# Optimization experiments

Measured on AMD Instinct MI355X. Metric: run time of the kernel, lower is better.

Reference implementation:

```python
import jax, jax.numpy as jnp
import numpy as np

B, N, F_IN, HID, OUT, NHEADS = 16, 1024, 64, 64, 64, 4
TAXI = 512        # get_Parameter('taxi_size') from the original repo (node split point)
ALPHA = 0.2       # LeakyReLU negative slope


def setup_inputs() -> dict:
    key = jax.random.key(0)
    ks = jax.random.split(key, 8)
    x = jax.random.normal(ks[0], (B, N, F_IN), dtype=jnp.float32)
    # multiplicative binary mask (mostly ones so softmax rows are well-conditioned)
    mask = (jax.random.uniform(ks[1], (N, N)) > 0.1).astype(jnp.float32)
    s_in = 1.0 / np.sqrt(F_IN)
    s_cat = 1.0 / np.sqrt(NHEADS * HID)
    W1 = jax.random.normal(ks[2], (NHEADS, F_IN, HID), jnp.float32) * s_in
    W2 = jax.random.normal(ks[3], (NHEADS, F_IN, HID), jnp.float32) * s_in
    a = jax.random.normal(ks[4], (NHEADS, 2 * HID), jnp.float32) * 0.1
    W1o = jax.random.normal(ks[5], (NHEADS * HID, OUT), jnp.float32) * s_cat
    W2o = jax.random.normal(ks[6], (NHEADS * HID, OUT), jnp.float32) * s_cat
    ao = jax.random.normal(ks[7], (2 * OUT,), jnp.float32) * 0.1
    return dict(x=x, mask=mask, W1=W1, W2=W2, a=a, W1o=W1o, W2o=W2o, ao=ao)


def _gat_layer(x, mask, W1, W2, a, out_dim):
    # x: [B,N,F]; W1,W2: [F,out_dim]; a: [2*out_dim]
    # node-group-split linear projection (taxi nodes via W1, rest via W2)
    h = jnp.concatenate([x[:, :TAXI] @ W1, x[:, TAXI:] @ W2], axis=1)  # [B,N,O]
    A1 = h @ a[:out_dim]                 # [B,N]
    A2 = h @ a[out_dim:]                 # [B,N]
    sim = A1[:, :, None] + A2[:, None, :]  # [B,N,N] additive scores
    e = jax.nn.leaky_relu(sim, ALPHA)
    e = mask[None, :, :] * e             # multiplicative mask (as in source)
    attn = jax.nn.softmax(e, axis=-1)    # [B,N,N]  (dropout omitted: eval mode)
    h_prime = jnp.einsum('bnm,bmo->bno', attn, h)
    return jax.nn.elu(h_prime), attn


def reference(x, mask, W1, W2, a, W1o, W2o, ao):
    # input dropout omitted (eval mode)
    heads = [_gat_layer(x, mask, W1[i], W2[i], a[i], HID)[0] for i in range(NHEADS)]
    xc = jnp.concatenate(heads, axis=-1)          # [B,N,NHEADS*HID]
    out, attn = _gat_layer(xc, mask, W1o, W2o, ao, OUT)
    return out, attn
```

## Files before the change

### kernel.cpp

```cpp
#include <hip/hip_runtime.h>
#include <hip/hip_bf16.h>

#define B_      16
#define N_      1024
#define ALPHA_  0.2f

typedef __attribute__((ext_vector_type(8))) __bf16 bf16x8;
typedef __attribute__((ext_vector_type(4))) float  floatx4;

__device__ __forceinline__ float eluf(float u) { return u > 0.f ? u : __expf(u) - 1.f; }

__device__ __forceinline__ floatx4 mfma_bf16(bf16x8 a, bf16x8 b, floatx4 c) {
    return __builtin_amdgcn_mfma_f32_16x16x32_bf16(a, b, c, 0, 0, 0);
}

__global__ __launch_bounds__(256) void maskbits_kernel(
    const float* __restrict__ mask, unsigned* __restrict__ bits)
{
    const int idx = blockIdx.x * 256 + threadIdx.x;
    const float* src = mask + (size_t)idx * 32;
    unsigned v = 0;
#pragma unroll
    for (int j = 0; j < 8; ++j) {
        float4 f = *(const float4*)(src + j * 4);
        v |= ((unsigned)(f.x != 0.f)) << (j * 4 + 0);
        v |= ((unsigned)(f.y != 0.f)) << (j * 4 + 1);
        v |= ((unsigned)(f.z != 0.f)) << (j * 4 + 2);
        v |= ((unsigned)(f.w != 0.f)) << (j * 4 + 3);
    }
    bits[idx] = v;
}

__global__ __launch_bounds__(256) void proj1_kernel(
    const float* __restrict__ x, const float* __restrict__ W1,
    const float* __restrict__ W2, const float* __restrict__ av,
    __bf16* __restrict__ h1t, float* __restrict__ A1, float* __restrict__ A2)
{
    const int tile = blockIdx.x, b = blockIdx.y, head = blockIdx.z;
    const int n0 = tile * 64;
    const float* W  = ((n0 < 512) ? W1 : W2) + head * 64 * 64;
    const float* ah = av + head * 128;

    __shared__ __align__(16) __bf16 xs[64][72];
    __shared__ __align__(16) __bf16 Wt[64][72];
    __shared__ __align__(16) float as_[128];

    const int tid = threadIdx.x;
    if (tid < 128) as_[tid] = ah[tid];
#pragma unroll
    for (int i = 0; i < 4; ++i) {
        int idx = i * 256 + tid;
        int r = idx >> 4, c = (idx & 15) * 4;
        float4 v = *(const float4*)(x + ((size_t)(b * N_ + n0 + r)) * 64 + c);
        xs[r][c+0] = (__bf16)v.x; xs[r][c+1] = (__bf16)v.y;
        xs[r][c+2] = (__bf16)v.z; xs[r][c+3] = (__bf16)v.w;
        float4 wv = *(const float4*)(W + (size_t)r * 64 + c);
        Wt[c+0][r] = (__bf16)wv.x; Wt[c+1][r] = (__bf16)wv.y;
        Wt[c+2][r] = (__bf16)wv.z; Wt[c+3][r] = (__bf16)wv.w;
    }
    __syncthreads();

    const int w = tid >> 6, L = tid & 63, quad = L >> 4, lo = L & 15;
    floatx4 acc[4] = {{0,0,0,0},{0,0,0,0},{0,0,0,0},{0,0,0,0}};
#pragma unroll
    for (int kc = 0; kc < 2; ++kc) {
        bf16x8 af = *(bf16x8*)&xs[16 * w + lo][kc * 32 + quad * 8];
#pragma unroll
        for (int t = 0; t < 4; ++t) {
            bf16x8 bv = *(bf16x8*)&Wt[16 * t + lo][kc * 32 + quad * 8];
            acc[t] = mfma_bf16(af, bv, acc[t]);
        }
    }

    float p1[4] = {0, 0, 0, 0}, p2[4] = {0, 0, 0, 0};
#pragma unroll
    for (int t = 0; t < 4; ++t) {
        float a1w = as_[16 * t + lo], a2w = as_[64 + 16 * t + lo];
#pragma unroll
        for (int i = 0; i < 4; ++i) { p1[i] += acc[t][i] * a1w; p2[i] += acc[t][i] * a2w; }
    }
#pragma unroll
    for (int s = 1; s < 16; s <<= 1)
#pragma unroll
        for (int i = 0; i < 4; ++i) {
            p1[i] += __shfl_xor(p1[i], s);
            p2[i] += __shfl_xor(p2[i], s);
        }
    const int bh = head * B_ + b;
    if (lo == 0) {
#pragma unroll
        for (int i = 0; i < 4; ++i) {
            int n = 16 * w + quad * 4 + i;
            A1[bh * N_ + n0 + n] = p1[i];
            A2[bh * N_ + n0 + n] = p2[i];
        }
    }

    __syncthreads();
#pragma unroll
    for (int t = 0; t < 4; ++t)
#pragma unroll
        for (int i = 0; i < 4; ++i)
            xs[16 * w + quad * 4 + i][16 * t + lo] = (__bf16)acc[t][i];
    __syncthreads();
    const int d = tid & 63, ch = tid >> 6;
    bf16x8 v0, v1;
#pragma unroll
    for (int j = 0; j < 8; ++j) v0[j] = xs[ch * 16 + j][d];
#pragma unroll
    for (int j = 0; j < 8; ++j) v1[j] = xs[ch * 16 + 8 + j][d];
    bf16x8* dst = (bf16x8*)(h1t + ((size_t)bh * 64 + d) * N_ + n0 + ch * 16);
    dst[0] = v0; dst[1] = v1;
}

__global__ __launch_bounds__(256, 4) void attn1_kernel(
    const float* __restrict__ A1g, const float* __restrict__ A2g,
    const __bf16* __restrict__ Htg, const unsigned* __restrict__ bitsG,
    __bf16* __restrict__ xc_out)
{
    const int b = blockIdx.x, head = blockIdx.y, tile = blockIdx.z;
    const int n0 = tile * 64;
    const int bh = head * B_ + b;
    const float* A2 = A2g + (size_t)bh * N_;
    const __bf16* Hglob = Htg + (size_t)bh * 64 * N_;

    __shared__ __align__(16) __bf16 Ht[2][64][72];
    __shared__ __align__(16) __bf16 ts[64][72];
    __shared__ __align__(16) float A2s[N_];
    __shared__ __align__(16) unsigned bitsS[2048];

    const int tid = threadIdx.x;
    *(float4*)&A2s[tid * 4] = *(const float4*)(A2 + tid * 4);
    {
        uint4 u0 = *(const uint4*)(bitsG + n0 * 32 + tid * 8);
        uint4 u1 = *(const uint4*)(bitsG + n0 * 32 + tid * 8 + 4);
        const int row = tid >> 2, wb0 = (tid & 3) * 8;
        bitsS[(wb0+0)*64+row] = u0.x; bitsS[(wb0+1)*64+row] = u0.y;
        bitsS[(wb0+2)*64+row] = u0.z; bitsS[(wb0+3)*64+row] = u0.w;
        bitsS[(wb0+4)*64+row] = u1.x; bitsS[(wb0+5)*64+row] = u1.y;
        bitsS[(wb0+6)*64+row] = u1.z; bitsS[(wb0+7)*64+row] = u1.w;
    }

    const int sr = tid >> 2, sq = tid & 3;
    const __bf16* hrow = Hglob + (size_t)sr * N_ + sq * 16;
    const int w = tid >> 6, L = tid & 63, quad = L >> 4, lo = L & 15;
    const int nloc = 16 * w + lo;
    const float a1r = A1g[(size_t)bh * N_ + n0 + nloc];
    const int shq = quad * 8;

    bf16x8 h0 = *(const bf16x8*)(hrow);
    bf16x8 h1 = *(const bf16x8*)(hrow + 8);
    *(bf16x8*)&Ht[0][sr][sq * 16]     = h0;
    *(bf16x8*)&Ht[0][sr][sq * 16 + 8] = h1;
    __syncthreads();

    floatx4 acc[4] = {{0,0,0,0},{0,0,0,0},{0,0,0,0},{0,0,0,0}};
    float zacc = 0.f;

    for (int mt = 0; mt < 16; ++mt) {
        const int cur = mt & 1;
        if (mt < 15) {
            h0 = *(const bf16x8*)(hrow + (mt + 1) * 64);
            h1 = *(const bf16x8*)(hrow + (mt + 1) * 64 + 8);
        }
        bf16x8 pf0, pf1;
#pragma unroll
        for (int kc = 0; kc < 2; ++kc) {
            const int mb = mt * 64 + kc * 32 + shq;
            const unsigned wbk = bitsS[(mt * 2 + kc) * 64 + nloc] >> shq;
            float4 alo = *(const float4*)&A2s[mb];
            float4 ahi = *(const float4*)&A2s[mb + 4];
            float a2v[8] = {alo.x, alo.y, alo.z, alo.w, ahi.x, ahi.y, ahi.z, ahi.w};
            float o[8];
#pragma unroll
            for (int j = 0; j < 8; ++j) {
                float s = a1r + a2v[j];
                float lr = fmaxf(s, ALPHA_ * s);
                int bm = (int)(wbk << (31 - j)) >> 31;
                lr = __int_as_float(__float_as_int(lr) & bm);
                float t = __expf(lr);
                zacc += t; o[j] = t;
            }
            bf16x8 pk = {(__bf16)o[0], (__bf16)o[1], (__bf16)o[2], (__bf16)o[3],
                         (__bf16)o[4], (__bf16)o[5], (__bf16)o[6], (__bf16)o[7]};
            if (kc == 0) pf0 = pk; else pf1 = pk;
        }
#pragma unroll
        for (int t = 0; t < 4; ++t) {
            bf16x8 bv = *(bf16x8*)&Ht[cur][16 * t + lo][shq];
            acc[t] = mfma_bf16(pf0, bv, acc[t]);
        }
#pragma unroll
        for (int t = 0; t < 4; ++t) {
            bf16x8 bv = *(bf16x8*)&Ht[cur][16 * t + lo][32 + shq];
            acc[t] = mfma_bf16(pf1, bv, acc[t]);
        }
        if (mt < 15) {
            *(bf16x8*)&Ht[cur ^ 1][sr][sq * 16]     = h0;
            *(bf16x8*)&Ht[cur ^ 1][sr][sq * 16 + 8] = h1;
            __syncthreads();
        }
    }

    zacc += __shfl_xor(zacc, 16);
    zacc += __shfl_xor(zacc, 32);
    const float invz = 1.f / zacc;
    float iz[4];
#pragma unroll
    for (int i = 0; i < 4; ++i) iz[i] = __shfl(invz, quad * 4 + i);

#pragma unroll
    for (int t = 0; t < 4; ++t)
#pragma unroll
        for (int i = 0; i < 4; ++i)
            ts[16 * w + quad * 4 + i][16 * t + lo] = (__bf16)eluf(acc[t][i] * iz[i]);
    __syncthreads();
#pragma unroll
    for (int i = 0; i < 2; ++i) {
        int cid = i * 256 + tid;
        int row = cid >> 3, c8 = (cid & 7) * 8;
        bf16x8 v = *(bf16x8*)&ts[row][c8];
        *(bf16x8*)(xc_out + ((size_t)(b * N_ + n0 + row)) * 256 + head * 64 + c8) = v;
    }
}

__global__ __launch_bounds__(256) void attn2_kernel(
    const float* __restrict__ A1g, const float* __restrict__ A2g,
    const __bf16* __restrict__ Htg, const unsigned* __restrict__ bitsG,
    float* __restrict__ out_f, float* __restrict__ attn_f)
{
    const int b = blockIdx.x, tile = blockIdx.z;
    const int n0 = tile * 32;
    const float* A2 = A2g + (size_t)b * N_;
    const __bf16* Hglob = Htg + (size_t)b * 64 * N_;

    __shared__ __align__(16) __bf16 ts2[2][32][72];
    __shared__ __align__(16) __bf16 Ht2[2][64][72];
    __shared__ __align__(16) float A2s[N_];
    __shared__ __align__(16) unsigned bitsS[1024];
    __shared__ float invz[32];

    const int tid = threadIdx.x;
    *(float4*)&A2s[tid * 4] = *(const float4*)(A2 + tid * 4);
    {
        uint4 u = *(const uint4*)(bitsG + n0 * 32 + tid * 4);
        const int row = tid >> 3, wb0 = (tid & 7) * 4;
        bitsS[(wb0+0)*32+row] = u.x; bitsS[(wb0+1)*32+row] = u.y;
        bitsS[(wb0+2)*32+row] = u.z; bitsS[(wb0+3)*32+row] = u.w;
    }

    const int r2 = tid >> 3, q2 = tid & 7;
    const float a1r = A1g[(size_t)b * N_ + n0 + r2];
    const int dr = tid >> 2, dq = tid & 3;
    const int w = tid >> 6, L = tid & 63, quad = L >> 4, lo = L & 15;
    const __bf16* hrow = Hglob + (size_t)dr * N_ + dq * 16;

    floatx4 acc2[2] = {{0,0,0,0},{0,0,0,0}};
    float zacc = 0.f;
    bf16x8 tr[16];

    __syncthreads();

    auto scores = [&](int mt) -> bf16x8 {
        const int mb = mt * 64 + q2 * 8;
        const unsigned wb = bitsS[(mt * 2 + (q2 >> 2)) * 32 + r2] >> ((q2 & 3) * 8);
        float4 alo = *(const float4*)&A2s[mb];
        float4 ahi = *(const float4*)&A2s[mb + 4];
        float a2v[8] = {alo.x, alo.y, alo.z, alo.w, ahi.x, ahi.y, ahi.z, ahi.w};
        float o[8];
#pragma unroll
        for (int j = 0; j < 8; ++j) {
            float s = a1r + a2v[j];
            float lr = fmaxf(s, ALPHA_ * s);
            int bm = (int)(wb << (31 - j)) >> 31;
            lr = __int_as_float(__float_as_int(lr) & bm);
            float t = __expf(lr);
            zacc += t; o[j] = t;
        }
        bf16x8 pk = {(__bf16)o[0], (__bf16)o[1], (__bf16)o[2], (__bf16)o[3],
                     (__bf16)o[4], (__bf16)o[5], (__bf16)o[6], (__bf16)o[7]};
        return pk;
    };

    {
        bf16x8 h0 = *(const bf16x8*)(hrow);
        bf16x8 h1 = *(const bf16x8*)(hrow + 8);
        bf16x8 pk = scores(0);
        tr[0] = pk;
        *(bf16x8*)&ts2[0][r2][q2 * 8]      = pk;
        *(bf16x8*)&Ht2[0][dr][dq * 16]     = h0;
        *(bf16x8*)&Ht2[0][dr][dq * 16 + 8] = h1;
    }
    __syncthreads();

#pragma unroll
    for (int mt = 0; mt < 16; ++mt) {
        const int cur = mt & 1;
        bf16x8 h0, h1, pk;
        if (mt < 15) {
            h0 = *(const bf16x8*)(hrow + (mt + 1) * 64);
            h1 = *(const bf16x8*)(hrow + (mt + 1) * 64 + 8);
            pk = scores(mt + 1);
            tr[mt + 1] = pk;
        }
#pragma unroll
        for (int c = 0; c < 2; ++c)
#pragma unroll
            for (int rt = 0; rt < 2; ++rt) {
                bf16x8 af = *(bf16x8*)&ts2[cur][16 * rt + lo][c * 32 + quad * 8];
                bf16x8 bv = *(bf16x8*)&Ht2[cur][16 * w + lo][c * 32 + quad * 8];
                acc2[rt] = mfma_bf16(af, bv, acc2[rt]);
            }
        if (mt < 15) {
            *(bf16x8*)&ts2[cur ^ 1][r2][q2 * 8]      = pk;
            *(bf16x8*)&Ht2[cur ^ 1][dr][dq * 16]     = h0;
            *(bf16x8*)&Ht2[cur ^ 1][dr][dq * 16 + 8] = h1;
            __syncthreads();
        }
    }

    zacc += __shfl_xor(zacc, 1);
    zacc += __shfl_xor(zacc, 2);
    zacc += __shfl_xor(zacc, 4);
    if (q2 == 0) invz[r2] = 1.f / zacc;
    __syncthreads();

#pragma unroll
    for (int rt = 0; rt < 2; ++rt)
#pragma unroll
        for (int i = 0; i < 4; ++i) {
            const int n = 16 * rt + quad * 4 + i;
            out_f[((size_t)(b * N_ + n0 + n)) * 64 + 16 * w + lo] =
                eluf(acc2[rt][i] * invz[n]);
        }

    const float iz = invz[r2];
    float* arow = attn_f + ((size_t)(b * N_ + n0 + r2)) * N_ + q2 * 8;
#pragma unroll
    for (int mt = 0; mt < 16; ++mt) {
        bf16x8 t8 = tr[mt];
        float4 f0 = make_float4((float)t8[0] * iz, (float)t8[1] * iz,
                                (float)t8[2] * iz, (float)t8[3] * iz);
        float4 f1 = make_float4((float)t8[4] * iz, (float)t8[5] * iz,
                                (float)t8[6] * iz, (float)t8[7] * iz);
        *(float4*)(arow + mt * 64)     = f0;
        *(float4*)(arow + mt * 64 + 4) = f1;
    }
}

__global__ __launch_bounds__(256) void proj2_kernel(
    const __bf16* __restrict__ xcb, const float* __restrict__ W1o,
    const float* __restrict__ W2o, const float* __restrict__ ao,
    __bf16* __restrict__ h2t, float* __restrict__ A1o, float* __restrict__ A2o)
{
    const int tile = blockIdx.x, b = blockIdx.y;
    const int n0 = tile * 64;
    const float* W = (n0 < 512) ? W1o : W2o;

    __shared__ __align__(16) __bf16 xs[64][264];
    __shared__ __align__(16) __bf16 Wt[64][264];
    __shared__ __align__(16) float as_[128];

    const int tid = threadIdx.x;
    if (tid < 128) as_[tid] = ao[tid];

#pragma unroll
    for (int i = 0; i < 8; ++i) {
        int idx = i * 256 + tid;
        int row = idx >> 5, c = (idx & 31) * 8;
        *(bf16x8*)&xs[row][c] =
            *(const bf16x8*)(xcb + ((size_t)(b * N_ + n0 + row)) * 256 + c);
    }
#pragma unroll
    for (int i = 0; i < 16; ++i) {
        int idx = i * 256 + tid;
        int k = idx >> 4, n4 = (idx & 15) * 4;
        float4 wv = *(const float4*)(W + (size_t)k * 64 + n4);
        Wt[n4 + 0][k] = (__bf16)wv.x;
        Wt[n4 + 1][k] = (__bf16)wv.y;
        Wt[n4 + 2][k] = (__bf16)wv.z;
        Wt[n4 + 3][k] = (__bf16)wv.w;
    }
    __syncthreads();

    const int w = tid >> 6, L = tid & 63, quad = L >> 4, lo = L & 15;
    floatx4 acc[4] = {{0,0,0,0},{0,0,0,0},{0,0,0,0},{0,0,0,0}};
#pragma unroll
    for (int kc = 0; kc < 8; ++kc) {
        bf16x8 af = *(bf16x8*)&xs[16 * w + lo][kc * 32 + quad * 8];
#pragma unroll
        for (int t = 0; t < 4; ++t) {
            bf16x8 bv = *(bf16x8*)&Wt[16 * t + lo][kc * 32 + quad * 8];
            acc[t] = mfma_bf16(af, bv, acc[t]);
        }
    }

    float p1[4] = {0, 0, 0, 0}, p2[4] = {0, 0, 0, 0};
#pragma unroll
    for (int t = 0; t < 4; ++t) {
        float a1w = as_[16 * t + lo], a2w = as_[64 + 16 * t + lo];
#pragma unroll
        for (int i = 0; i < 4; ++i) { p1[i] += acc[t][i] * a1w; p2[i] += acc[t][i] * a2w; }
    }
#pragma unroll
    for (int s = 1; s < 16; s <<= 1)
#pragma unroll
        for (int i = 0; i < 4; ++i) {
            p1[i] += __shfl_xor(p1[i], s);
            p2[i] += __shfl_xor(p2[i], s);
        }
    if (lo == 0) {
#pragma unroll
        for (int i = 0; i < 4; ++i) {
            int n = 16 * w + quad * 4 + i;
            A1o[b * N_ + n0 + n] = p1[i];
            A2o[b * N_ + n0 + n] = p2[i];
        }
    }

    __syncthreads();
#pragma unroll
    for (int t = 0; t < 4; ++t)
#pragma unroll
        for (int i = 0; i < 4; ++i)
            xs[16 * w + quad * 4 + i][16 * t + lo] = (__bf16)acc[t][i];
    __syncthreads();
    const int d = tid & 63, ch = tid >> 6;
    bf16x8 v0, v1;
#pragma unroll
    for (int j = 0; j < 8; ++j) v0[j] = xs[ch * 16 + j][d];
#pragma unroll
    for (int j = 0; j < 8; ++j) v1[j] = xs[ch * 16 + 8 + j][d];
    bf16x8* dst = (bf16x8*)(h2t + ((size_t)b * 64 + d) * N_ + n0 + ch * 16);
    dst[0] = v0; dst[1] = v1;
}

extern "C" void kernel_launch(void* const* d_in, const int* in_sizes, int n_in,
                              void* d_out, int out_size, void* d_ws, size_t ws_size,
                              hipStream_t stream)
{
    const float* x    = (const float*)d_in[0];
    const float* mask = (const float*)d_in[1];
    const float* W1   = (const float*)d_in[2];
    const float* W2   = (const float*)d_in[3];
    const float* a    = (const float*)d_in[4];
    const float* W1o  = (const float*)d_in[5];
    const float* W2o  = (const float*)d_in[6];
    const float* ao   = (const float*)d_in[7];

    float* out      = (float*)d_out;
    float* attn_out = out + (size_t)B_ * N_ * 64;

    float*    ws    = (float*)d_ws;
    float*    A1    = ws;
    float*    A2    = A1 + 65536;
    float*    A1o   = A2 + 65536;
    float*    A2o   = A1o + 16384;
    __bf16*   h1t   = (__bf16*)(A2o + 16384);
    __bf16*   h2t   = h1t + 4194304;
    __bf16*   xcb   = h2t + 1048576;
    unsigned* bitsG = (unsigned*)(xcb + 4194304);

    maskbits_kernel<<<dim3(128), 256, 0, stream>>>(mask, bitsG);
    proj1_kernel<<<dim3(16, 16, 4), 256, 0, stream>>>(x, W1, W2, a, h1t, A1, A2);
    attn1_kernel<<<dim3(16, 4, 16), 256, 0, stream>>>(A1, A2, h1t, bitsG, xcb);
    proj2_kernel<<<dim3(16, 16, 1), 256, 0, stream>>>(xcb, W1o, W2o, ao, h2t, A1o, A2o);
    attn2_kernel<<<dim3(16, 1, 32), 256, 0, stream>>>(A1o, A2o, h2t, bitsG, out, attn_out);
}
```

Baseline: 153.8 us.

## Use 32x32 MFMA with 128-row tiles in attn1, fold maskbits into proj1, use exp2

Rewrites the first attention kernel to process 128 query rows per block using 32x32x16 bf16 MFMA with a fragment-ordered shared-memory layout for H, halving the grid in z and reducing redundant H loads per output row. The mask-to-bits conversion is fused into proj1, which removes one kernel launch. Scores are prescaled by log2(e) so a native exp2 can replace __expf. The risks are lower occupancy from the larger tile and the removed launch-bounds hint, and the fused mask bits relying on proj1's grid mapping exactly onto the bit array.

```diff
diff --git a/kernel.cpp b/kernel.cpp
--- a/kernel.cpp
+++ b/kernel.cpp
@@ -4,36 +4,33 @@
 #define B_      16
 #define N_      1024
 #define ALPHA_  0.2f
-
-typedef __attribute__((ext_vector_type(8))) __bf16 bf16x8;
-typedef __attribute__((ext_vector_type(4))) float  floatx4;
+#define LOG2E_  1.4426950408889634f
+
+typedef __attribute__((ext_vector_type(8)))  __bf16 bf16x8;
+typedef __attribute__((ext_vector_type(4)))  float  floatx4;
+typedef __attribute__((ext_vector_type(16))) float  floatx16;
 
 __device__ __forceinline__ float eluf(float u) { return u > 0.f ? u : __expf(u) - 1.f; }
+
+__device__ __forceinline__ float exp2fast(float x) {
+#if __has_builtin(__builtin_amdgcn_exp2f)
+    return __builtin_amdgcn_exp2f(x);
+#else
+    return exp2f(x);
+#endif
+}
 
 __device__ __forceinline__ floatx4 mfma_bf16(bf16x8 a, bf16x8 b, floatx4 c) {
     return __builtin_amdgcn_mfma_f32_16x16x32_bf16(a, b, c, 0, 0, 0);
 }
-
-__global__ __launch_bounds__(256) void maskbits_kernel(
-    const float* __restrict__ mask, unsigned* __restrict__ bits)
-{
-    const int idx = blockIdx.x * 256 + threadIdx.x;
-    const float* src = mask + (size_t)idx * 32;
-    unsigned v = 0;
-#pragma unroll
-    for (int j = 0; j < 8; ++j) {
-        float4 f = *(const float4*)(src + j * 4);
-        v |= ((unsigned)(f.x != 0.f)) << (j * 4 + 0);
-        v |= ((unsigned)(f.y != 0.f)) << (j * 4 + 1);
-        v |= ((unsigned)(f.z != 0.f)) << (j * 4 + 2);
-        v |= ((unsigned)(f.w != 0.f)) << (j * 4 + 3);
-    }
-    bits[idx] = v;
+__device__ __forceinline__ floatx16 mfma32_bf16(bf16x8 a, bf16x8 b, floatx16 c) {
+    return __builtin_amdgcn_mfma_f32_32x32x16_bf16(a, b, c, 0, 0, 0);
 }
 
 __global__ __launch_bounds__(256) void proj1_kernel(
     const float* __restrict__ x, const float* __restrict__ W1,
     const float* __restrict__ W2, const float* __restrict__ av,
+    const float* __restrict__ maskG, unsigned* __restrict__ bitsOut,
     __bf16* __restrict__ h1t, float* __restrict__ A1, float* __restrict__ A2)
 {
     const int tile = blockIdx.x, b = blockIdx.y, head = blockIdx.z;
@@ -58,6 +55,23 @@
         Wt[c+0][r] = (__bf16)wv.x; Wt[c+1][r] = (__bf16)wv.y;
         Wt[c+2][r] = (__bf16)wv.z; Wt[c+3][r] = (__bf16)wv.w;
     }
+
+    {
+        const int bid = blockIdx.x + 16 * (blockIdx.y + 16 * blockIdx.z);
+        if (tid < 32) {
+            const float* src = maskG + ((size_t)(bid * 32 + tid)) * 32;
+            unsigned v = 0;
+#pragma unroll
+            for (int j = 0; j < 8; ++j) {
+                float4 f = *(const float4*)(src + j * 4);
+                v |= ((unsigned)(f.x != 0.f)) << (j * 4 + 0);
+                v |= ((unsigned)(f.y != 0.f)) << (j * 4 + 1);
+                v |= ((unsigned)(f.z != 0.f)) << (j * 4 + 2);
+                v |= ((unsigned)(f.w != 0.f)) << (j * 4 + 3);
+            }
+            bitsOut[bid * 32 + tid] = v;
+        }
+    }
     __syncthreads();
 
     const int w = tid >> 6, L = tid & 63, quad = L >> 4, lo = L & 15;
@@ -91,8 +105,8 @@
 #pragma unroll
         for (int i = 0; i < 4; ++i) {
             int n = 16 * w + quad * 4 + i;
-            A1[bh * N_ + n0 + n] = p1[i];
-            A2[bh * N_ + n0 + n] = p2[i];
+            A1[bh * N_ + n0 + n] = p1[i] * LOG2E_;
+            A2[bh * N_ + n0 + n] = p2[i] * LOG2E_;
         }
     }
 
@@ -113,48 +127,55 @@
     dst[0] = v0; dst[1] = v1;
 }
 
-__global__ __launch_bounds__(256, 4) void attn1_kernel(
+__global__ __launch_bounds__(256) void attn1_kernel(
     const float* __restrict__ A1g, const float* __restrict__ A2g,
     const __bf16* __restrict__ Htg, const unsigned* __restrict__ bitsG,
     __bf16* __restrict__ xc_out)
 {
     const int b = blockIdx.x, head = blockIdx.y, tile = blockIdx.z;
-    const int n0 = tile * 64;
+    const int n0 = tile * 128;
     const int bh = head * B_ + b;
     const float* A2 = A2g + (size_t)bh * N_;
     const __bf16* Hglob = Htg + (size_t)bh * 64 * N_;
 
-    __shared__ __align__(16) __bf16 Ht[2][64][72];
-    __shared__ __align__(16) __bf16 ts[64][72];
+    __shared__ __align__(16) __bf16 frag[2][4][2][64][8];
+    __shared__ __align__(16) __bf16 ts[128][72];
     __shared__ __align__(16) float A2s[N_];
-    __shared__ __align__(16) unsigned bitsS[2048];
+    __shared__ __align__(16) unsigned bitsS[32 * 128];
+    __shared__ float invzS[128];
 
     const int tid = threadIdx.x;
     *(float4*)&A2s[tid * 4] = *(const float4*)(A2 + tid * 4);
     {
-        uint4 u0 = *(const uint4*)(bitsG + n0 * 32 + tid * 8);
-        uint4 u1 = *(const uint4*)(bitsG + n0 * 32 + tid * 8 + 4);
-        const int row = tid >> 2, wb0 = (tid & 3) * 8;
-        bitsS[(wb0+0)*64+row] = u0.x; bitsS[(wb0+1)*64+row] = u0.y;
-        bitsS[(wb0+2)*64+row] = u0.z; bitsS[(wb0+3)*64+row] = u0.w;
-        bitsS[(wb0+4)*64+row] = u1.x; bitsS[(wb0+5)*64+row] = u1.y;
-        bitsS[(wb0+6)*64+row] = u1.z; bitsS[(wb0+7)*64+row] = u1.w;
-    }
-
-    const int sr = tid >> 2, sq = tid & 3;
-    const __bf16* hrow = Hglob + (size_t)sr * N_ + sq * 16;
-    const int w = tid >> 6, L = tid & 63, quad = L >> 4, lo = L & 15;
-    const int nloc = 16 * w + lo;
-    const float a1r = A1g[(size_t)bh * N_ + n0 + nloc];
-    const int shq = quad * 8;
+        const int row = tid >> 1, w0 = (tid & 1) * 16;
+        uint4 u0 = *(const uint4*)(bitsG + n0 * 32 + tid * 16);
+        uint4 u1 = *(const uint4*)(bitsG + n0 * 32 + tid * 16 + 4);
+        uint4 u2 = *(const uint4*)(bitsG + n0 * 32 + tid * 16 + 8);
+        uint4 u3 = *(const uint4*)(bitsG + n0 * 32 + tid * 16 + 12);
+        bitsS[(w0+ 0)*128+row] = u0.x; bitsS[(w0+ 1)*128+row] = u0.y;
+        bitsS[(w0+ 2)*128+row] = u0.z; bitsS[(w0+ 3)*128+row] = u0.w;
+        bitsS[(w0+ 4)*128+row] = u1.x; bitsS[(w0+ 5)*128+row] = u1.y;
+        bitsS[(w0+ 6)*128+row] = u1.z; bitsS[(w0+ 7)*128+row] = u1.w;
+        bitsS[(w0+ 8)*128+row] = u2.x; bitsS[(w0+ 9)*128+row] = u2.y;
+        bitsS[(w0+10)*128+row] = u2.z; bitsS[(w0+11)*128+row] = u2.w;
+        bitsS[(w0+12)*128+row] = u3.x; bitsS[(w0+13)*128+row] = u3.y;
+        bitsS[(w0+14)*128+row] = u3.z; bitsS[(w0+15)*128+row] = u3.w;
+    }
+
+    const int sd = tid >> 2, sq = tid & 3;
+    const __bf16* hrow = Hglob + (size_t)sd * N_ + sq * 16;
+    const int L = tid & 63, rg = tid >> 6, hi = L >> 5, lq = L & 31;
+    const int rloc = rg * 32 + lq;
+    const float a1r = A1g[(size_t)bh * N_ + n0 + rloc];
 
     bf16x8 h0 = *(const bf16x8*)(hrow);
     bf16x8 h1 = *(const bf16x8*)(hrow + 8);
-    *(bf16x8*)&Ht[0][sr][sq * 16]     = h0;
-    *(bf16x8*)&Ht[0][sr][sq * 16 + 8] = h1;
-    __syncthreads();
-
-    floatx4 acc[4] = {{0,0,0,0},{0,0,0,0},{0,0,0,0},{0,0,0,0}};
+    *(bf16x8*)&frag[0][sq][sd >> 5][(sd & 31)][0]      = h0;
+    *(bf16x8*)&frag[0][sq][sd >> 5][(sd & 31) + 32][0] = h1;
+    __syncthreads();
+
+    floatx16 acc0 = {0,0,0,0,0,0,0,0,0,0,0,0,0,0,0,0};
+    floatx16 acc1 = {0,0,0,0,0,0,0,0,0,0,0,0,0,0,0,0};
     float zacc = 0.f;
 
     for (int mt = 0; mt < 16; ++mt) {
@@ -163,60 +184,55 @@
             h0 = *(const bf16x8*)(hrow + (mt + 1) * 64);
             h1 = *(const bf16x8*)(hrow + (mt + 1) * 64 + 8);
         }
-        bf16x8 pf0, pf1;
-#pragma unroll
-        for (int kc = 0; kc < 2; ++kc) {
-            const int mb = mt * 64 + kc * 32 + shq;
-            const unsigned wbk = bitsS[(mt * 2 + kc) * 64 + nloc] >> shq;
-            float4 alo = *(const float4*)&A2s[mb];
-            float4 ahi = *(const float4*)&A2s[mb + 4];
-            float a2v[8] = {alo.x, alo.y, alo.z, alo.w, ahi.x, ahi.y, ahi.z, ahi.w};
+#pragma unroll
+        for (int ks = 0; ks < 4; ++ks) {
+            const int mbase = mt * 64 + ks * 16 + hi * 8;
+            const unsigned wb = bitsS[(mbase >> 5) * 128 + rloc] >> (mbase & 31);
+            float4 av  = *(const float4*)&A2s[mbase];
+            float4 av2 = *(const float4*)&A2s[mbase + 4];
+            float a2v[8] = {av.x, av.y, av.z, av.w, av2.x, av2.y, av2.z, av2.w};
             float o[8];
 #pragma unroll
             for (int j = 0; j < 8; ++j) {
                 float s = a1r + a2v[j];
                 float lr = fmaxf(s, ALPHA_ * s);
-                int bm = (int)(wbk << (31 - j)) >> 31;
+                int bm = (int)(wb << (31 - j)) >> 31;
                 lr = __int_as_float(__float_as_int(lr) & bm);
-                float t = __expf(lr);
+                float t = exp2fast(lr);
                 zacc += t; o[j] = t;
             }
-            bf16x8 pk = {(__bf16)o[0], (__bf16)o[1], (__bf16)o[2], (__bf16)o[3],
+            bf16x8 af = {(__bf16)o[0], (__bf16)o[1], (__bf16)o[2], (__bf16)o[3],
                          (__bf16)o[4], (__bf16)o[5], (__bf16)o[6], (__bf16)o[7]};
-            if (kc == 0) pf0 = pk; else pf1 = pk;
-        }
-#pragma unroll
-        for (int t = 0; t < 4; ++t) {
-            bf16x8 bv = *(bf16x8*)&Ht[cur][16 * t + lo][shq];
-            acc[t] = mfma_bf16(pf0, bv, acc[t]);
-        }
-#pragma unroll
-        for (int t = 0; t < 4; ++t) {
-            bf16x8 bv = *(bf16x8*)&Ht[cur][16 * t + lo][32 + shq];
-            acc[t] = mfma_bf16(pf1, bv, acc[t]);
+            bf16x8 bv0 = *(bf16x8*)&frag[cur][ks][0][L][0];
+            bf16x8 bv1 = *(bf16x8*)&frag[cur][ks][1][L][0];
+            acc0 = mfma32_bf16(af, bv0, acc0);
+            acc1 = mfma32_bf16(af, bv1, acc1);
         }
         if (mt < 15) {
-            *(bf16x8*)&Ht[cur ^ 1][sr][sq * 16]     = h0;
-            *(bf16x8*)&Ht[cur ^ 1][sr][sq * 16 + 8] = h1;
+            *(bf16x8*)&frag[cur ^ 1][sq][sd >> 5][(sd & 31)][0]      = h0;
+            *(bf16x8*)&frag[cur ^ 1][sq][sd >> 5][(sd & 31) + 32][0] = h1;
             __syncthreads();
         }
     }
 
-    zacc += __shfl_xor(zacc, 16);
     zacc += __shfl_xor(zacc, 32);
-    const float invz = 1.f / zacc;
-    float iz[4];
-#pragma unroll
-    for (int i = 0; i < 4; ++i) iz[i] = __shfl(invz, quad * 4 + i);
-
-#pragma unroll
-    for (int t = 0; t < 4; ++t)
-#pragma unroll
-        for (int i = 0; i < 4; ++i)
-            ts[16 * w + quad * 4 + i][16 * t + lo] = (__bf16)eluf(acc[t][i] * iz[i]);
-    __syncthreads();
-#pragma unroll
-    for (int i = 0; i < 2; ++i) {
+    if (hi == 0) invzS[rloc] = 1.f / zacc;
+    __syncthreads();
+
+    float iz[16];
+#pragma unroll
+    for (int r = 0; r < 16; ++r)
+        iz[r] = invzS[rg * 32 + (r & 3) + 8 * (r >> 2) + 4 * hi];
+
+#pragma unroll
+    for (int r = 0; r < 16; ++r) {
+        const int row = rg * 32 + (r & 3) + 8 * (r >> 2) + 4 * hi;
+        ts[row][lq]      = (__bf16)eluf(acc0[r] * iz[r]);
+        ts[row][32 + lq] = (__bf16)eluf(acc1[r] * iz[r]);
+    }
+    __syncthreads();
+#pragma unroll
+    for (int i = 0; i < 4; ++i) {
         int cid = i * 256 + tid;
         int row = cid >> 3, c8 = (cid & 7) * 8;
         bf16x8 v = *(bf16x8*)&ts[row][c8];
@@ -274,7 +290,7 @@
             float lr = fmaxf(s, ALPHA_ * s);
             int bm = (int)(wb << (31 - j)) >> 31;
             lr = __int_as_float(__float_as_int(lr) & bm);
-            float t = __expf(lr);
+            float t = exp2fast(lr);
             zacc += t; o[j] = t;
         }
         bf16x8 pk = {(__bf16)o[0], (__bf16)o[1], (__bf16)o[2], (__bf16)o[3],
@@ -413,8 +429,8 @@
 #pragma unroll
         for (int i = 0; i < 4; ++i) {
             int n = 16 * w + quad * 4 + i;
-            A1o[b * N_ + n0 + n] = p1[i];
-            A2o[b * N_ + n0 + n] = p2[i];
+            A1o[b * N_ + n0 + n] = p1[i] * LOG2E_;
+            A2o[b * N_ + n0 + n] = p2[i] * LOG2E_;
         }
     }
 
@@ -461,9 +477,9 @@
     __bf16*   xcb   = h2t + 1048576;
     unsigned* bitsG = (unsigned*)(xcb + 4194304);
 
-    maskbits_kernel<<<dim3(128), 256, 0, stream>>>(mask, bitsG);
-    proj1_kernel<<<dim3(16, 16, 4), 256, 0, stream>>>(x, W1, W2, a, h1t, A1, A2);
-    attn1_kernel<<<dim3(16, 4, 16), 256, 0, stream>>>(A1, A2, h1t, bitsG, xcb);
+    proj1_kernel<<<dim3(16, 16, 4), 256, 0, stream>>>(x, W1, W2, a, mask, bitsG,
+                                                      h1t, A1, A2);
+    attn1_kernel<<<dim3(16, 4, 8), 256, 0, stream>>>(A1, A2, h1t, bitsG, xcb);
     proj2_kernel<<<dim3(16, 16, 1), 256, 0, stream>>>(xcb, W1o, W2o, ao, h2t, A1o, A2o);
     attn2_kernel<<<dim3(16, 1, 32), 256, 0, stream>>>(A1o, A2o, h2t, bitsG, out, attn_out);
 }
```

Result: faster. 150.0 us (median of 2 runs) (-2.5%).
